# Performance work log

Hardware: AMD Instinct MI355X
Metric: run time of the kernel (lower is better)

The kernel has to match this reference:

```python
import jax, jax.numpy as jnp
import numpy as np

N_A, N_P, E = 50000, 50000, 600000
H, D = 8, 16
C = H * D  # hidden_channels = 128
OUT = 16
F_A, F_P = 256, 128
NEG_SLOPE = 0.2
EPS = 1e-5


def setup_inputs():
    key = jax.random.key(0)
    ks = jax.random.split(key, 16)
    return {
        'x_author': jax.random.normal(ks[0], (N_A, F_A), jnp.float32),
        'x_paper': jax.random.normal(ks[1], (N_P, F_P), jnp.float32),
        'W_a': jax.random.normal(ks[2], (F_A, C), jnp.float32) / np.sqrt(F_A).astype(np.float32),
        'b_a': jnp.zeros((C,), jnp.float32),
        'W_p': jax.random.normal(ks[3], (F_P, C), jnp.float32) / np.sqrt(F_P).astype(np.float32),
        'b_p': jnp.zeros((C,), jnp.float32),
        'att_src_ap': jax.random.normal(ks[4], (H, D), jnp.float32) * 0.1,
        'att_dst_ap': jax.random.normal(ks[5], (H, D), jnp.float32) * 0.1,
        'att_src_pp': jax.random.normal(ks[6], (H, D), jnp.float32) * 0.1,
        'att_dst_pp': jax.random.normal(ks[7], (H, D), jnp.float32) * 0.1,
        'k_W': jax.random.normal(ks[8], (C, C), jnp.float32) / np.sqrt(C).astype(np.float32),
        'k_b': jnp.zeros((C,), jnp.float32),
        'q': jax.random.normal(ks[9], (C,), jnp.float32) * 0.1,
        'norm_w': jnp.ones((C,), jnp.float32),
        'norm_b': jnp.zeros((C,), jnp.float32),
        'norm_ms': jnp.ones((C,), jnp.float32),
        'lin_W': jax.random.normal(ks[10], (C, OUT), jnp.float32) / np.sqrt(C).astype(np.float32),
        'lin_b': jnp.zeros((OUT,), jnp.float32),
        'edge_ap': jax.random.randint(ks[11], (2, E), 0, N_A),
        'edge_pp': jax.random.randint(ks[12], (2, E), 0, N_P),
    }


def _edge_type_out(h_src, h_dst, edge, a_src, a_dst, n_dst):
    # Node-level attention for one edge type (PyG HANConv per-metapath GAT).
    alpha_s = jnp.einsum('nhd,hd->nh', h_src, a_src)  # [N_src, H]
    alpha_d = jnp.einsum('nhd,hd->nh', h_dst, a_dst)  # [N_dst, H]
    src, dst = edge[0], edge[1]
    alpha = alpha_s[src] + alpha_d[dst]                       # [E, H]
    alpha = jnp.where(alpha >= 0, alpha, NEG_SLOPE * alpha)   # leaky_relu(0.2)
    m = jax.ops.segment_max(alpha, dst, num_segments=n_dst)
    e = jnp.exp(alpha - m[dst])
    denom = jax.ops.segment_sum(e, dst, num_segments=n_dst)
    attn = e / denom[dst]                                     # softmax over incoming edges
    msg = h_src[src] * attn[:, :, None]                       # [E, H, D]
    out = jax.ops.segment_sum(msg, dst, num_segments=n_dst)   # [n_dst, H, D]
    return jax.nn.relu(out.reshape(n_dst, H * D))


def reference(x_author, x_paper, W_a, b_a, W_p, b_p, att_src_ap, att_dst_ap,
              att_src_pp, att_dst_pp, k_W, k_b, q, norm_w, norm_b, norm_ms,
              lin_W, lin_b, edge_ap, edge_pp):
    # per-node-type projections -> [N, H, D]
    h_a = (x_author @ W_a + b_a).reshape(N_A, H, D)
    h_p = (x_paper @ W_p + b_p).reshape(N_P, H, D)
    # per-edge-type node-level attention + aggregation (both target 'paper')
    out_ap = _edge_type_out(h_a, h_p, edge_ap, att_src_ap, att_dst_ap, N_P)
    out_pp = _edge_type_out(h_p, h_p, edge_pp, att_src_pp, att_dst_pp, N_P)
    # semantic-level attention across the R=2 meta-paths
    outs = jnp.stack([out_ap, out_pp], axis=0)               # [R, N_P, C]
    w = jnp.tanh(outs @ k_W + k_b).mean(axis=1) @ q          # [R]
    beta = jax.nn.softmax(w)
    out = jnp.einsum('rnc,r->nc', outs, beta)                # [N_P, C]
    # GraphNorm (single graph: stats over all nodes)
    mean = out.mean(axis=0)
    o = out - mean * norm_ms
    var = (o * o).mean(axis=0)
    o = norm_w * o / jnp.sqrt(var + EPS) + norm_b
    # final classifier
    return o @ lin_W + lin_b
```

## Files before the change

### kernel.cpp

```cpp
#include <hip/hip_runtime.h>
#include <math.h>

#define NN   50000
#define EE   600000
#define CCH  128
#define HH   8
#define DD   16
#define OUTC 16
#define NEG  0.2f
#define EPSN 1e-5f
#define SCHUNKS 1172
#define CAP 64
#define SBKT 32

typedef _Float16 f16x8 __attribute__((ext_vector_type(8)));
typedef float    f32x4 __attribute__((ext_vector_type(4)));

__device__ __forceinline__ float fast_tanh(float x) {
    x = fminf(10.f, fmaxf(-10.f, x));
    float e = __expf(2.f * x);
    return (e - 1.f) / (e + 1.f);
}

__device__ __forceinline__ float lrelu(float x) {
    return (x >= 0.f) ? x : NEG * x;
}

__global__ __launch_bounds__(256) void convw_k(const float* __restrict__ W_a,
        const float* __restrict__ W_p, const float* __restrict__ k_W,
        const float* __restrict__ lin_W, _Float16* __restrict__ Wt_a,
        _Float16* __restrict__ Wt_p, _Float16* __restrict__ kWt,
        _Float16* __restrict__ linWt)
{
    int id = blockIdx.x * 256 + threadIdx.x;
    if (id < 32768) {
        int k = id >> 7, n = id & 127;
        Wt_a[n * 256 + k] = (_Float16)W_a[id];
    } else if (id < 49152) {
        int i = id - 32768; int k = i >> 7, n = i & 127;
        Wt_p[n * 128 + k] = (_Float16)W_p[i];
    } else if (id < 65536) {
        int i = id - 49152; int k = i >> 7, n = i & 127;
        kWt[n * 128 + k] = (_Float16)k_W[i];
    } else if (id < 67584) {
        int i = id - 65536; int k = i >> 4, n = i & 15;
        linWt[n * 128 + k] = (_Float16)lin_W[i];
    }
}

__global__ __launch_bounds__(256) void gemm_k(const float* __restrict__ X_a,
        const float* __restrict__ X_p, const _Float16* __restrict__ Wt_a,
        const _Float16* __restrict__ Wt_p, const float* __restrict__ b_a,
        const float* __restrict__ b_p,
        const float* __restrict__ att_s_ap, const float* __restrict__ att_d_ap,
        const float* __restrict__ att_s_pp, const float* __restrict__ att_d_pp,
        _Float16* __restrict__ h_a, _Float16* __restrict__ h_p,
        _Float16* __restrict__ as_ap, _Float16* __restrict__ ad_ap,
        _Float16* __restrict__ as_pp, _Float16* __restrict__ ad_pp,
        int GBn)
{
    __shared__ _Float16 ldsbuf[8704];
    _Float16 (*As)[40]  = (_Float16(*)[40])ldsbuf;
    _Float16 (*Bs)[40]  = (_Float16(*)[40])(ldsbuf + 2560);
    _Float16 (*Cs)[136] = (_Float16(*)[136])ldsbuf;
    const int t = threadIdx.x;
    const int gb = (int)blockIdx.x;
    const int which = (gb >= GBn) ? 1 : 0;
    const float* X = which ? X_p : X_a;
    const _Float16* Wt = which ? Wt_p : Wt_a;
    const float* bias = which ? b_p : b_a;
    _Float16* Y = which ? h_p : h_a;
    const int K = which ? 128 : 256;
    const int r0 = (gb - which * GBn) * 64;
    const int lane = t & 63;
    const int wv = t >> 6;
    const int m16 = lane & 15;
    const int kq = lane >> 4;
    f32x4 acc[8];
#pragma unroll
    for (int i = 0; i < 8; ++i) acc[i] = (f32x4){0.f, 0.f, 0.f, 0.f};

    const int ar = t >> 2;
    const int ak = (t & 3) * 8;
    const int br = t >> 1;
    const int bk = (t & 1) * 16;

    for (int kc = 0; kc < K; kc += 32) {
        int row = r0 + ar;
        f16x8 av;
        if (row < NN) {
            const float4* gp = (const float4*)&X[row * K + kc + ak];
            float4 x0 = gp[0], x1 = gp[1];
            av[0] = (_Float16)x0.x; av[1] = (_Float16)x0.y;
            av[2] = (_Float16)x0.z; av[3] = (_Float16)x0.w;
            av[4] = (_Float16)x1.x; av[5] = (_Float16)x1.y;
            av[6] = (_Float16)x1.z; av[7] = (_Float16)x1.w;
        } else {
#pragma unroll
            for (int j = 0; j < 8; ++j) av[j] = (_Float16)0.f;
        }
        *(f16x8*)&As[ar][ak] = av;
        const f16x8* wp = (const f16x8*)&Wt[br * K + kc + bk];
        *(f16x8*)&Bs[br][bk]     = wp[0];
        *(f16x8*)&Bs[br][bk + 8] = wp[1];
        __syncthreads();
        f16x8 af = *(const f16x8*)&As[wv * 16 + m16][kq * 8];
#pragma unroll
        for (int i = 0; i < 8; ++i) {
            f16x8 bf = *(const f16x8*)&Bs[i * 16 + m16][kq * 8];
            acc[i] = __builtin_amdgcn_mfma_f32_16x16x32_f16(af, bf, acc[i], 0, 0, 0);
        }
        __syncthreads();
    }
    const int rbase = r0 + wv * 16 + kq * 4;
#pragma unroll
    for (int i = 0; i < 8; ++i) {
        int col = i * 16 + m16;
        float bv = bias[col];
        float hv[4];
#pragma unroll
        for (int rr = 0; rr < 4; ++rr) hv[rr] = acc[i][rr] + bv;
#pragma unroll
        for (int rr = 0; rr < 4; ++rr)
            Cs[wv * 16 + kq * 4 + rr][col] = (_Float16)hv[rr];
        if (which == 0) {
            float av = att_s_ap[col];
            float p[4];
#pragma unroll
            for (int rr = 0; rr < 4; ++rr) p[rr] = hv[rr] * av;
#pragma unroll
            for (int x = 1; x < 16; x <<= 1)
#pragma unroll
                for (int rr = 0; rr < 4; ++rr) p[rr] += __shfl_xor(p[rr], x, 64);
            if (m16 == 0) {
#pragma unroll
                for (int rr = 0; rr < 4; ++rr)
                    if (rbase + rr < NN) as_ap[(rbase + rr) * 8 + i] = (_Float16)p[rr];
            }
        } else {
            float a1 = att_d_ap[col];
            float a2 = att_s_pp[col];
            float a3 = att_d_pp[col];
            float p1[4], p2[4], p3[4];
#pragma unroll
            for (int rr = 0; rr < 4; ++rr) {
                p1[rr] = hv[rr] * a1; p2[rr] = hv[rr] * a2; p3[rr] = hv[rr] * a3;
            }
#pragma unroll
            for (int x = 1; x < 16; x <<= 1) {
#pragma unroll
                for (int rr = 0; rr < 4; ++rr) {
                    p1[rr] += __shfl_xor(p1[rr], x, 64);
                    p2[rr] += __shfl_xor(p2[rr], x, 64);
                    p3[rr] += __shfl_xor(p3[rr], x, 64);
                }
            }
            if (m16 == 0) {
#pragma unroll
                for (int rr = 0; rr < 4; ++rr) {
                    if (rbase + rr < NN) {
                        ad_ap[(rbase + rr) * 8 + i] = (_Float16)p1[rr];
                        as_pp[(rbase + rr) * 8 + i] = (_Float16)p2[rr];
                        ad_pp[(rbase + rr) * 8 + i] = (_Float16)p3[rr];
                    }
                }
            }
        }
    }
    __syncthreads();
    {
        int row = t >> 2;
        int gr = r0 + row;
        if (gr < NN) {
            int colblk = (t & 3) * 32;
#pragma unroll
            for (int i = 0; i < 4; ++i) {
                int c0 = colblk + i * 8;
                *(f16x8*)&Y[(size_t)gr * CCH + c0] = *(const f16x8*)&Cs[row][c0];
            }
        }
    }
}

__global__ __launch_bounds__(256) void scat_k(const int* __restrict__ ea,
        const int* __restrict__ ep, int* __restrict__ fill, int* __restrict__ csrp)
{
    const int t = threadIdx.x;
    int base = (int)blockIdx.x * 1024 + t;
    int d[4];
#pragma unroll
    for (int it = 0; it < 4; ++it) {
        int e = base + it * 256;
        int dd = -1;
        if (e < EE) dd = ea[EE + e];
        else if (e < 2 * EE) dd = NN + ep[e];
        d[it] = dd;
    }
#pragma unroll
    for (int it = 0; it < 4; ++it) {
        int dd = d[it];
        if (dd >= 0) {
            int e = base + it * 256;
            int pos = atomicAdd(&fill[dd], 1);
            if (pos < CAP) {
                int s = (e < EE) ? ea[e] : ep[e - EE];
                csrp[(size_t)dd * CAP + pos] = s;
            }
        }
    }
}

__device__ __forceinline__ void agg_path(
        const _Float16* __restrict__ hsrc, const _Float16* __restrict__ as,
        float adv, int cnt, const int* __restrict__ row, int h, int sub,
        float* acc, float& l)
{
    int4 r0 = *(const int4*)&row[0];
    int4 r1 = *(const int4*)&row[4];
    int4 r2 = *(const int4*)&row[8];
    int4 r3 = *(const int4*)&row[12];
    int s[16] = {r0.x, r0.y, r0.z, r0.w, r1.x, r1.y, r1.z, r1.w,
                 r2.x, r2.y, r2.z, r2.w, r3.x, r3.y, r3.z, r3.w};
#pragma unroll
    for (int e = 0; e < 16; ++e) s[e] = (e < cnt) ? s[e] : 0;
    float av[16];
#pragma unroll
    for (int e = 0; e < 16; ++e) av[e] = (float)as[s[e] * 8 + h];
    f16x8 hv[16];
#pragma unroll
    for (int e = 0; e < 16; ++e)
        hv[e] = *(const f16x8*)&hsrc[(size_t)s[e] * CCH + sub * 8];
#pragma unroll
    for (int e = 0; e < 16; ++e) {
        float w = (e < cnt) ? __expf(lrelu(av[e] + adv)) : 0.f;
        l += w;
#pragma unroll
        for (int i = 0; i < 8; ++i) acc[i] += w * (float)hv[e][i];
    }
    if (cnt > 16) {
        int4 r4 = *(const int4*)&row[16];
        int4 r5 = *(const int4*)&row[20];
        int s2[8] = {r4.x, r4.y, r4.z, r4.w, r5.x, r5.y, r5.z, r5.w};
#pragma unroll
        for (int e = 0; e < 8; ++e) s2[e] = (16 + e < cnt) ? s2[e] : 0;
        float av2[8];
#pragma unroll
        for (int e = 0; e < 8; ++e) av2[e] = (float)as[s2[e] * 8 + h];
        f16x8 hv2[8];
#pragma unroll
        for (int e = 0; e < 8; ++e)
            hv2[e] = *(const f16x8*)&hsrc[(size_t)s2[e] * CCH + sub * 8];
#pragma unroll
        for (int e = 0; e < 8; ++e) {
            float w = (16 + e < cnt) ? __expf(lrelu(av2[e] + adv)) : 0.f;
            l += w;
#pragma unroll
            for (int i = 0; i < 8; ++i) acc[i] += w * (float)hv2[e][i];
        }
        for (int p = 24; p < cnt; ++p) {
            int s0 = row[p];
            float w = __expf(lrelu((float)as[s0 * 8 + h] + adv));
            f16x8 v = *(const f16x8*)&hsrc[(size_t)s0 * CCH + sub * 8];
            l += w;
#pragma unroll
            for (int i = 0; i < 8; ++i) acc[i] += w * (float)v[i];
        }
    }
}

__global__ __launch_bounds__(256) void agg4f_k(
        const _Float16* __restrict__ h_a, const _Float16* __restrict__ h_p,
        const _Float16* __restrict__ as_ap, const _Float16* __restrict__ ad_ap,
        const _Float16* __restrict__ as_pp, const _Float16* __restrict__ ad_pp,
        const int* __restrict__ fill, const int* __restrict__ csrp,
        const _Float16* __restrict__ kWt, const float* __restrict__ kb,
        const float* __restrict__ qv,
        _Float16* __restrict__ out_ap, _Float16* __restrict__ out_pp,
        float* __restrict__ wacc, float* __restrict__ statsb)
{
    __shared__ _Float16 Aap[16][136];
    __shared__ _Float16 App[16][136];
    __shared__ float wred[4];
    const int t = threadIdx.x;
    const int wave = t >> 6, lane = t & 63;
    const int q = lane >> 4, sub = lane & 15;
    const int pw = wave >> 1;
    const int slot = (wave & 1) * 4 + q;
    const int n = blockIdx.x * 8 + slot;
    const int h = sub >> 1;
    {
        _Float16* za = &Aap[8][0];
        _Float16* zb = &App[8][0];
        for (int i = t; i < 8 * 136; i += 256) {
            za[i] = (_Float16)0.f; zb[i] = (_Float16)0.f;
        }
    }
    const _Float16* hsrc = pw ? h_p : h_a;
    const _Float16* as   = pw ? as_pp : as_ap;
    const _Float16* ad   = pw ? ad_pp : ad_ap;
    const int gnode = pw ? NN + n : n;
    float adv = (float)ad[n * 8 + h];
    int cnt = fill[gnode]; if (cnt > CAP) cnt = CAP;
    const int* row = &csrp[(size_t)gnode * CAP];
    float l = 0.f;
    float acc[8] = {0.f,0.f,0.f,0.f,0.f,0.f,0.f,0.f};

    agg_path(hsrc, as, adv, cnt, row, h, sub, acc, l);

    float inv = (l > 0.f) ? 1.f / l : 0.f;
    f16x8 vo;
#pragma unroll
    for (int i = 0; i < 8; ++i) vo[i] = (_Float16)fmaxf(acc[i] * inv, 0.f);
    if (pw == 0) {
        *(f16x8*)&out_ap[n * CCH + sub * 8] = vo;
        *(f16x8*)&Aap[slot][sub * 8] = vo;
    } else {
        *(f16x8*)&out_pp[n * CCH + sub * 8] = vo;
        *(f16x8*)&App[slot][sub * 8] = vo;
    }
    __syncthreads();
    const int m16 = lane & 15, kq = lane >> 4;
    float local = 0.f;
#pragma unroll
    for (int j = 0; j < 4; ++j) {
        int ct = (wave & 1) * 4 + j;
        f32x4 acc2 = (f32x4){0.f, 0.f, 0.f, 0.f};
#pragma unroll
        for (int kc = 0; kc < 128; kc += 32) {
            f16x8 af = pw ? *(const f16x8*)&App[m16][kc + kq * 8]
                          : *(const f16x8*)&Aap[m16][kc + kq * 8];
            f16x8 bf = *(const f16x8*)&kWt[(ct * 16 + m16) * 128 + kc + kq * 8];
            acc2 = __builtin_amdgcn_mfma_f32_16x16x32_f16(af, bf, acc2, 0, 0, 0);
        }
        if (kq < 2) {
            float kbc = kb[ct * 16 + m16], qc = qv[ct * 16 + m16];
#pragma unroll
            for (int rr = 0; rr < 4; ++rr)
                local += fast_tanh(acc2[rr] + kbc) * qc;
        }
    }
#pragma unroll
    for (int x = 1; x < 64; x <<= 1) local += __shfl_xor(local, x, 64);
    if (lane == 0) wred[wave] = local;
    __syncthreads();
    if (t == 0) atomicAdd(&wacc[(blockIdx.x & 15) * 16],       wred[0] + wred[1]);
    if (t == 1) atomicAdd(&wacc[256 + (blockIdx.x & 15) * 16], wred[2] + wred[3]);
    if (t < 128) {
        int c = t;
        float vsa = 0.f, vsb = 0.f, vssa = 0.f, vssb = 0.f, vsab = 0.f;
#pragma unroll
        for (int r = 0; r < 8; ++r) {
            float a = (float)Aap[r][c];
            float b = (float)App[r][c];
            vsa += a; vsb += b; vssa += a * a; vssb += b * b; vsab += a * b;
        }
        float* sp = statsb + (size_t)(blockIdx.x & (SBKT - 1)) * 128;
        atomicAdd(&sp[c],                vsa);
        atomicAdd(&sp[SBKT*128 + c],     vsb);
        atomicAdd(&sp[2*SBKT*128 + c],   vssa);
        atomicAdd(&sp[3*SBKT*128 + c],   vssb);
        atomicAdd(&sp[4*SBKT*128 + c],   vsab);
    }
}

__global__ __launch_bounds__(256) void final2_k(
        const _Float16* __restrict__ oa, const _Float16* __restrict__ ob,
        const float* __restrict__ wacc, const float* __restrict__ statsb,
        const float* __restrict__ ms, const float* __restrict__ nw,
        const float* __restrict__ nb,
        const _Float16* __restrict__ linWt, const float* __restrict__ linb,
        float* __restrict__ out)
{
    __shared__ _Float16 As[64][136];
    __shared__ float scl[128], shf[128];
    __shared__ float bcoef[2];
    int t = threadIdx.x;
    if (t < 128) {
        float w0s = 0.f, w1s = 0.f;
#pragma unroll
        for (int i = 0; i < 16; ++i) {
            w0s += wacc[i * 16];
            w1s += wacc[256 + i * 16];
        }
        float w0 = w0s * (1.f / NN), w1 = w1s * (1.f / NN);
        float mm = fmaxf(w0, w1);
        float e0 = __expf(w0 - mm), e1 = __expf(w1 - mm);
        float b0 = e0 / (e0 + e1), b1 = e1 / (e0 + e1);
        if (t == 0) { bcoef[0] = b0; bcoef[1] = b1; }
        int c = t;
        float vsA = 0.f, vsB = 0.f, vssA = 0.f, vssB = 0.f, vsAB = 0.f;
        for (int i = 0; i < SBKT; ++i) {
            vsA  += statsb[i * 128 + c];
            vsB  += statsb[SBKT*128 + i * 128 + c];
            vssA += statsb[2*SBKT*128 + i * 128 + c];
            vssB += statsb[3*SBKT*128 + i * 128 + c];
            vsAB += statsb[4*SBKT*128 + i * 128 + c];
        }
        float mean = (b0 * vsA + b1 * vsB) * (1.f / NN);
        float ex2 = (b0 * b0 * vssA + 2.f * b0 * b1 * vsAB + b1 * b1 * vssB) * (1.f / NN);
        float a = mean * ms[c];
        float var = ex2 - 2.f * a * mean + a * a;
        float sc = nw[c] * rsqrtf(var + EPSN);
        scl[c] = sc;
        shf[c] = nb[c] - a * sc;
    }
    __syncthreads();
    float b0 = bcoef[0], b1 = bcoef[1];
    int r0 = blockIdx.x * 64;
    int row = t >> 2, cp = (t & 3) * 32;
    int gr = r0 + row;
    if (gr < NN) {
#pragma unroll
        for (int i = 0; i < 4; ++i) {
            int c0 = cp + i * 8;
            f16x8 va = *(const f16x8*)&oa[gr * CCH + c0];
            f16x8 vb = *(const f16x8*)&ob[gr * CCH + c0];
            f16x8 o;
#pragma unroll
            for (int e2 = 0; e2 < 8; ++e2) {
                float v = b0 * (float)va[e2] + b1 * (float)vb[e2];
                o[e2] = (_Float16)(v * scl[c0 + e2] + shf[c0 + e2]);
            }
            *(f16x8*)&As[row][c0] = o;
        }
    } else {
        f16x8 z;
#pragma unroll
        for (int e2 = 0; e2 < 8; ++e2) z[e2] = (_Float16)0.f;
#pragma unroll
        for (int i = 0; i < 4; ++i) *(f16x8*)&As[row][cp + i * 8] = z;
    }
    __syncthreads();
    int lane = t & 63, wv = t >> 6;
    int m16 = lane & 15, kq = lane >> 4;
    f32x4 acc = (f32x4){0.f, 0.f, 0.f, 0.f};
#pragma unroll
    for (int kc = 0; kc < 128; kc += 32) {
        f16x8 af = *(const f16x8*)&As[wv * 16 + m16][kc + kq * 8];
        f16x8 bf = *(const f16x8*)&linWt[m16 * 128 + kc + kq * 8];
        acc = __builtin_amdgcn_mfma_f32_16x16x32_f16(af, bf, acc, 0, 0, 0);
    }
    float lb = linb[m16];
#pragma unroll
    for (int r = 0; r < 4; ++r) {
        int gr2 = r0 + wv * 16 + kq * 4 + r;
        if (gr2 < NN) out[gr2 * 16 + m16] = acc[r] + lb;
    }
}

extern "C" void kernel_launch(void* const* d_in, const int* in_sizes, int n_in,
                              void* d_out, int out_size, void* d_ws, size_t ws_size,
                              hipStream_t stream) {
    const float* x_a   = (const float*)d_in[0];
    const float* x_p   = (const float*)d_in[1];
    const float* W_a   = (const float*)d_in[2];
    const float* b_a   = (const float*)d_in[3];
    const float* W_p   = (const float*)d_in[4];
    const float* b_p   = (const float*)d_in[5];
    const float* att_src_ap = (const float*)d_in[6];
    const float* att_dst_ap = (const float*)d_in[7];
    const float* att_src_pp = (const float*)d_in[8];
    const float* att_dst_pp = (const float*)d_in[9];
    const float* k_W   = (const float*)d_in[10];
    const float* k_b   = (const float*)d_in[11];
    const float* q     = (const float*)d_in[12];
    const float* norm_w = (const float*)d_in[13];
    const float* norm_b = (const float*)d_in[14];
    const float* norm_ms = (const float*)d_in[15];
    const float* lin_W = (const float*)d_in[16];
    const float* lin_b = (const float*)d_in[17];
    const int* edge_ap = (const int*)d_in[18];
    const int* edge_pp = (const int*)d_in[19];
    float* out = (float*)d_out;

    char* base = (char*)d_ws;
    size_t off = 0;
    auto alloc = [&](size_t bytes) -> void* {
        void* r = base + off;
        off += (bytes + 255) & ~(size_t)255;
        return r;
    };
    _Float16* h_a    = (_Float16*)alloc((size_t)NN * CCH * 2);
    _Float16* h_p    = (_Float16*)alloc((size_t)NN * CCH * 2);
    _Float16* out_ap = (_Float16*)alloc((size_t)NN * CCH * 2);
    _Float16* out_pp = (_Float16*)alloc((size_t)NN * CCH * 2);
    _Float16* as_ap  = (_Float16*)alloc((size_t)NN * HH * 2);
    _Float16* ad_ap  = (_Float16*)alloc((size_t)NN * HH * 2);
    _Float16* as_pp  = (_Float16*)alloc((size_t)NN * HH * 2);
    _Float16* ad_pp  = (_Float16*)alloc((size_t)NN * HH * 2);
    _Float16* Wt_a = (_Float16*)alloc((size_t)128 * 256 * 2);
    _Float16* Wt_p = (_Float16*)alloc((size_t)128 * 128 * 2);
    _Float16* kWt  = (_Float16*)alloc((size_t)128 * 128 * 2);
    _Float16* linWt = (_Float16*)alloc((size_t)16 * 128 * 2);
    int* csrp = (int*)alloc((size_t)2 * NN * CAP * 4);
    const size_t ZCOUNT = 100000 + 512 + 5 * SBKT * 128;
    int* zz = (int*)alloc(ZCOUNT * 4);
    int* fill   = zz;
    float* wacc = (float*)(zz + 100000);
    float* statsb = (float*)(zz + 100512);

    (void)in_sizes; (void)n_in; (void)out_size; (void)ws_size;

    hipMemsetAsync(zz, 0, ZCOUNT * 4, stream);

    convw_k<<<264, 256, 0, stream>>>(W_a, W_p, k_W, lin_W, Wt_a, Wt_p, kWt, linWt);

    const int GB = (NN + 63) / 64;
    gemm_k<<<2 * GB, 256, 0, stream>>>(
        x_a, x_p, Wt_a, Wt_p, b_a, b_p,
        att_src_ap, att_dst_ap, att_src_pp, att_dst_pp,
        h_a, h_p, as_ap, ad_ap, as_pp, ad_pp, GB);

    scat_k<<<SCHUNKS, 256, 0, stream>>>(edge_ap, edge_pp, fill, csrp);

    agg4f_k<<<NN / 8, 256, 0, stream>>>(h_a, h_p, as_ap, ad_ap, as_pp, ad_pp,
                                        fill, csrp, kWt, k_b, q,
                                        out_ap, out_pp, wacc, statsb);

    final2_k<<<GB, 256, 0, stream>>>(out_ap, out_pp, wacc, statsb,
                                     norm_ms, norm_w, norm_b, linWt, lin_b, out);
}
```

Before: 389.8 us.

## Fuse edge scatter into GEMM launch and pad fill counters

Edge-bucketing scatter blocks are appended to the GEMM grid, so the CSR build runs concurrently with the projection GEMM instead of as a separate launch. The per-node fill counters are padded to one counter per 64 bytes to reduce atomic contention and false sharing. This costs a much larger zeroing memset and sparser counter reads in the aggregation kernel.

```diff
diff --git a/kernel.cpp b/kernel.cpp
--- a/kernel.cpp
+++ b/kernel.cpp
@@ -11,6 +11,7 @@
 #define EPSN 1e-5f
 #define SCHUNKS 1172
 #define CAP 64
+#define FS  16
 #define SBKT 32
 
 typedef _Float16 f16x8 __attribute__((ext_vector_type(8)));
@@ -48,7 +49,7 @@
     }
 }
 
-__global__ __launch_bounds__(256) void gemm_k(const float* __restrict__ X_a,
+__global__ __launch_bounds__(256) void gemm2h_k(const float* __restrict__ X_a,
         const float* __restrict__ X_p, const _Float16* __restrict__ Wt_a,
         const _Float16* __restrict__ Wt_p, const float* __restrict__ b_a,
         const float* __restrict__ b_p,
@@ -57,13 +58,40 @@
         _Float16* __restrict__ h_a, _Float16* __restrict__ h_p,
         _Float16* __restrict__ as_ap, _Float16* __restrict__ ad_ap,
         _Float16* __restrict__ as_pp, _Float16* __restrict__ ad_pp,
-        int GBn)
+        const int* __restrict__ ea, const int* __restrict__ ep,
+        int* __restrict__ fill, int* __restrict__ csrp, int GBn)
 {
     __shared__ _Float16 ldsbuf[8704];
     _Float16 (*As)[40]  = (_Float16(*)[40])ldsbuf;
     _Float16 (*Bs)[40]  = (_Float16(*)[40])(ldsbuf + 2560);
     _Float16 (*Cs)[136] = (_Float16(*)[136])ldsbuf;
     const int t = threadIdx.x;
+    if ((int)blockIdx.x >= 2 * GBn) {
+        int bb = (int)blockIdx.x - 2 * GBn;
+        int base = bb * 1024 + t;
+        int d[4];
+#pragma unroll
+        for (int it = 0; it < 4; ++it) {
+            int e = base + it * 256;
+            int dd = -1;
+            if (e < EE) dd = ea[EE + e];
+            else if (e < 2 * EE) dd = NN + ep[e];
+            d[it] = dd;
+        }
+#pragma unroll
+        for (int it = 0; it < 4; ++it) {
+            int dd = d[it];
+            if (dd >= 0) {
+                int e = base + it * 256;
+                int pos = atomicAdd(&fill[(size_t)dd * FS], 1);
+                if (pos < CAP) {
+                    int s = (e < EE) ? ea[e] : ep[e - EE];
+                    csrp[(size_t)dd * CAP + pos] = s;
+                }
+            }
+        }
+        return;
+    }
     const int gb = (int)blockIdx.x;
     const int which = (gb >= GBn) ? 1 : 0;
     const float* X = which ? X_p : X_a;
@@ -177,34 +205,6 @@
             for (int i = 0; i < 4; ++i) {
                 int c0 = colblk + i * 8;
                 *(f16x8*)&Y[(size_t)gr * CCH + c0] = *(const f16x8*)&Cs[row][c0];
-            }
-        }
-    }
-}
-
-__global__ __launch_bounds__(256) void scat_k(const int* __restrict__ ea,
-        const int* __restrict__ ep, int* __restrict__ fill, int* __restrict__ csrp)
-{
-    const int t = threadIdx.x;
-    int base = (int)blockIdx.x * 1024 + t;
-    int d[4];
-#pragma unroll
-    for (int it = 0; it < 4; ++it) {
-        int e = base + it * 256;
-        int dd = -1;
-        if (e < EE) dd = ea[EE + e];
-        else if (e < 2 * EE) dd = NN + ep[e];
-        d[it] = dd;
-    }
-#pragma unroll
-    for (int it = 0; it < 4; ++it) {
-        int dd = d[it];
-        if (dd >= 0) {
-            int e = base + it * 256;
-            int pos = atomicAdd(&fill[dd], 1);
-            if (pos < CAP) {
-                int s = (e < EE) ? ea[e] : ep[e - EE];
-                csrp[(size_t)dd * CAP + pos] = s;
             }
         }
     }
@@ -300,7 +300,7 @@
     const _Float16* ad   = pw ? ad_pp : ad_ap;
     const int gnode = pw ? NN + n : n;
     float adv = (float)ad[n * 8 + h];
-    int cnt = fill[gnode]; if (cnt > CAP) cnt = CAP;
+    int cnt = fill[(size_t)gnode * FS]; if (cnt > CAP) cnt = CAP;
     const int* row = &csrp[(size_t)gnode * CAP];
     float l = 0.f;
     float acc[8] = {0.f,0.f,0.f,0.f,0.f,0.f,0.f,0.f};
@@ -493,11 +493,11 @@
     _Float16* kWt  = (_Float16*)alloc((size_t)128 * 128 * 2);
     _Float16* linWt = (_Float16*)alloc((size_t)16 * 128 * 2);
     int* csrp = (int*)alloc((size_t)2 * NN * CAP * 4);
-    const size_t ZCOUNT = 100000 + 512 + 5 * SBKT * 128;
+    const size_t ZCOUNT = (size_t)2 * NN * FS + 512 + 5 * SBKT * 128;
     int* zz = (int*)alloc(ZCOUNT * 4);
     int* fill   = zz;
-    float* wacc = (float*)(zz + 100000);
-    float* statsb = (float*)(zz + 100512);
+    float* wacc = (float*)(zz + 2 * NN * FS);
+    float* statsb = (float*)(zz + 2 * NN * FS + 512);
 
     (void)in_sizes; (void)n_in; (void)out_size; (void)ws_size;
 
@@ -506,12 +506,11 @@
     convw_k<<<264, 256, 0, stream>>>(W_a, W_p, k_W, lin_W, Wt_a, Wt_p, kWt, linWt);
 
     const int GB = (NN + 63) / 64;
-    gemm_k<<<2 * GB, 256, 0, stream>>>(
+    gemm2h_k<<<2 * GB + SCHUNKS, 256, 0, stream>>>(
         x_a, x_p, Wt_a, Wt_p, b_a, b_p,
         att_src_ap, att_dst_ap, att_src_pp, att_dst_pp,
-        h_a, h_p, as_ap, ad_ap, as_pp, ad_pp, GB);
-
-    scat_k<<<SCHUNKS, 256, 0, stream>>>(edge_ap, edge_pp, fill, csrp);
+        h_a, h_p, as_ap, ad_ap, as_pp, ad_pp,
+        edge_ap, edge_pp, fill, csrp, GB);
 
     agg4f_k<<<NN / 8, 256, 0, stream>>>(h_a, h_p, as_ap, ad_ap, as_pp, ad_pp,
                                         fill, csrp, kWt, k_b, q,
```

After: 337.4 us. 1.16x faster.
